# Optimization experiments

Measured on AMD Instinct MI355X. Metric: run time of the kernel, lower is better.

## Reference

```python
import jax, jax.numpy as jnp
import numpy as np
import math

B, C, H, W = 32, 256, 56, 56
M = 16            # num_frequency_mixtures
MIX = 4           # sqrt(M)
K = 8             # num_fourier_basis + 1
HID = 16
STRIDE = (1, 1)
EPS = 1e-5


def setup_inputs() -> dict:
    key = jax.random.key(0)
    ks = jax.random.split(key, 8)
    return {
        "x": jax.random.normal(ks[0], (B, C, H, W), jnp.float32),
        "fc1_w": jax.random.normal(ks[1], (HID, C), jnp.float32) * 0.08,
        "fc1_b": jnp.zeros((HID,), jnp.float32),
        "ln_g": jnp.ones((HID,), jnp.float32),
        "ln_b": jnp.zeros((HID,), jnp.float32),
        "fh_w": jax.random.normal(ks[2], (C * M * K, HID), jnp.float32) * 0.08,
        "fh_b": jnp.zeros((C * M * K,), jnp.float32),
        "basis_real": jax.random.normal(ks[3], (K, 56, 32), jnp.float32) * 0.5,
        "basis_imag": jax.random.normal(ks[4], (K, 56, 32), jnp.float32) * 0.5,
        "conv_w": jax.random.normal(ks[5], (C, C), jnp.float32) * (1.0 / math.sqrt(C)),
        "bn_g": jnp.ones((C,), jnp.float32),
        "bn_b": jnp.zeros((C,), jnp.float32),
    }


def reference(x, fc1_w, fc1_b, ln_g, ln_b, fh_w, fh_b,
              basis_real, basis_imag, conv_w, bn_g, bn_b):
    b, c, h, w = x.shape
    # --- FrequencyAttention: GAP -> fc1 -> LN -> ReLU -> fourier_head ---
    ctx = x.mean(axis=(2, 3))                          # (B, C)
    hdn = ctx @ fc1_w.T + fc1_b                        # (B, HID)
    mu = hdn.mean(-1, keepdims=True)
    var = hdn.var(-1, keepdims=True)
    hdn = (hdn - mu) / jnp.sqrt(var + EPS) * ln_g + ln_b
    hdn = jax.nn.relu(hdn)
    att = hdn @ fh_w.T + fh_b                          # (B, C*M*K)

    coeffs = jax.nn.softmax(att.reshape(b, c, M, K), axis=-1)  # (B,C,M,K)

    # --- work-canvas sizes ---
    h_out, w_out = h // STRIDE[0], w // STRIDE[1]
    h_work = math.ceil(h / MIX) * MIX                  # 56
    w_f = w // 2 + 1                                   # 29
    w_f_work = math.ceil(w_f / MIX) * MIX              # 32
    w_work = (w_f_work - 1) * 2 if w_f_work > 1 else 1 # 62

    if (h_work, w_work) != (h, w):
        x_work = jax.image.resize(x, (b, c, h_work, w_work), "bilinear")
    else:
        x_work = x

    x_ft = jnp.fft.rfft2(x_work, s=(h_work, w_work), norm="ortho")  # (B,C,Hw,Wfw) complex
    wf = x_ft.shape[-1]                                # == w_f_work
    ph, pwf = h_work // MIX, wf // MIX                 # 14, 8

    basis = jax.lax.complex(basis_real, basis_imag)    # (K, Hw, Wfw)
    basis_p = basis.reshape(K, MIX, ph, MIX, pwf).transpose(1, 3, 0, 2, 4)
    basis_p = basis_p.reshape(M, K, ph, pwf)           # (M,K,ph,pwf)

    x_ft_p = x_ft.reshape(b, c, MIX, ph, MIX, pwf).transpose(0, 2, 4, 1, 3, 5)
    x_ft_p = x_ft_p.reshape(b, M, c, ph, pwf)          # (B,M,C,ph,pwf)

    coeffs_c = jax.lax.complex(coeffs, jnp.zeros_like(coeffs))
    coeffs_p = coeffs_c.transpose(0, 2, 1, 3)          # (B,M,C,K)

    kernel = jnp.einsum("bmck,mkhw->bmchw", coeffs_p, basis_p)  # (B,M,C,ph,pwf)
    out_ft_p = x_ft_p * kernel

    out_ft = out_ft_p.reshape(b, MIX, MIX, c, ph, pwf).transpose(0, 3, 1, 4, 2, 5)
    out_ft = out_ft.reshape(b, c, h_work, wf)

    s_work = (h_work // STRIDE[0], w_work // STRIDE[1])
    y = jnp.fft.irfft2(out_ft, s=s_work, norm="ortho")  # (B,C,56,62)

    if y.shape[2:] != (h_out, w_out):
        y = jax.image.resize(y, (b, c, h_out, w_out), "bilinear")

    # --- 1x1 conv + BatchNorm (batch statistics, training-mode math) ---
    y = jnp.einsum("bchw,oc->bohw", y, conv_w)
    m = y.mean(axis=(0, 2, 3))
    v = y.var(axis=(0, 2, 3))
    y = (y - m[None, :, None, None]) / jnp.sqrt(v + EPS)[None, :, None, None]
    y = y * bn_g[None, :, None, None] + bn_b[None, :, None, None]
    return y
```

## Files before the change

### kernel.cpp

```cpp
#include <hip/hip_runtime.h>
#include <math.h>

typedef __attribute__((ext_vector_type(4))) float f32x4;
typedef __attribute__((ext_vector_type(8))) short s16x8;
typedef __attribute__((ext_vector_type(4))) short s16x4;
typedef unsigned short ushort_t;

#define MFMA16(a, b, c) __builtin_amdgcn_mfma_f32_16x16x32_bf16((a), (b), (c), 0, 0, 0)

#define WO_CTX    0u
#define WO_HDN    32768u
#define WO_BNSUM  34816u
#define WO_BNSQ   35840u
#define WO_SCALE  36864u
#define WO_SHIFT  37888u
#define WO_COEF   40960u
#define WO_BMT_H  4235264u
#define WO_BMT_L  4243456u
#define WO_FARE_H 4251648u
#define WO_FARE_L 4268032u
#define WO_FAIM_H 4284416u
#define WO_FAIM_L 4300800u
#define WO_FDRE_H 4317184u
#define WO_FDRE_L 4333568u
#define WO_FDIM_H 4349952u
#define WO_FDIM_L 4366336u
#define WO_DTT_H  4382720u
#define WO_DTT_L  4390912u
#define WO_CW_H   4399104u
#define WO_CW_L   4530176u
#define WO_YBF    4661248u
#define WO_BASRT  56041472u
#define WO_BASIT  56098816u

__device__ __forceinline__ ushort_t f2bf(float f) {
  unsigned int u = __builtin_bit_cast(unsigned int, f);
  unsigned int r = (u + 0x7fffu + ((u >> 16) & 1u)) >> 16;
  return (ushort_t)r;
}
__device__ __forceinline__ float bf2f(ushort_t h) {
  unsigned int u = ((unsigned int)h) << 16;
  return __builtin_bit_cast(float, u);
}

__device__ double bmat_val(int w, int vv) {
  const int v = vv & 31;
  const bool isI = vv >= 32;
  double accR = 0.0, accI = 0.0;
  for (int wp = 0; wp < 62; ++wp) {
    const double src = (wp + 0.5) * (56.0 / 62.0) - 0.5;
    const int w0 = (int)floor(src);
    const double f = src - (double)w0;
    const double s0 = (w0 >= 0 && w0 <= 55) ? (1.0 - f) : 0.0;
    const double s1 = (w0 + 1 >= 0 && w0 + 1 <= 55) ? f : 0.0;
    const double ssum = s0 + s1;
    double wgt = 0.0;
    if (w == w0) wgt = s0 / ssum;
    else if (w == w0 + 1) wgt = s1 / ssum;
    if (wgt != 0.0) {
      const int p = (v * wp) % 62;
      const double ang = 6.283185307179586476925286766559 * (double)p / 62.0;
      accR += wgt * cos(ang);
      accI -= wgt * sin(ang);
    }
  }
  const double nrm = 1.0 / sqrt(3472.0);
  return (isI ? accI : accR) * nrm;
}

__device__ double dt_component(int v, bool isI, int wq) {
  const double ks = 62.0 / 56.0;
  const double src = (wq + 0.5) * ks - 0.5;
  double wsum = 0.0;
  for (int wp = 0; wp < 62; ++wp) {
    const double xx = fabs(src - (double)wp) / ks;
    if (xx < 1.0) wsum += 1.0 - xx;
  }
  const double cv = (v == 0 || v == 31) ? 1.0 : 2.0;
  double accR = 0.0, accI = 0.0;
  for (int wp = 0; wp < 62; ++wp) {
    const double xx = fabs(src - (double)wp) / ks;
    if (xx >= 1.0) continue;
    const double wgt = (1.0 - xx) / wsum;
    double cc, ss;
    if (v == 0)       { cc = 1.0; ss = 0.0; }
    else if (v == 31) { cc = (wp & 1) ? -1.0 : 1.0; ss = 0.0; }
    else {
      const int p = (v * wp) % 62;
      const double ang = 6.283185307179586476925286766559 * (double)p / 62.0;
      cc = cos(ang); ss = sin(ang);
    }
    accR += wgt * cv * cc;
    accI -= wgt * cv * ss;
  }
  const double nrm = 1.0 / sqrt(3472.0);
  return (isI ? accI : accR) * nrm;
}

__device__ __forceinline__ void emit_hilo(ushort_t* hp, ushort_t* lp, int off, double val) {
  const float fv = (float)val;
  const ushort_t h = f2bf(fv);
  const float hf = bf2f(h);
  const ushort_t l = f2bf((float)(val - (double)hf));
  hp[off] = h;
  lp[off] = l;
}

__global__ void k_const(const float* __restrict__ conv_w,
                        const float* __restrict__ basR, const float* __restrict__ basI,
                        ushort_t* BmT_h, ushort_t* BmT_l,
                        ushort_t* FARe_h, ushort_t* FARe_l,
                        ushort_t* FAIm_h, ushort_t* FAIm_l,
                        ushort_t* FDRe_h, ushort_t* FDRe_l,
                        ushort_t* FDIm_h, ushort_t* FDIm_l,
                        ushort_t* DtT_h, ushort_t* DtT_l,
                        ushort_t* W_h, ushort_t* W_l,
                        float* basRT, float* basIT) {
  const int idx = blockIdx.x * 256 + threadIdx.x;
  if (idx < 4096) {
    const int vv = idx >> 6, k = idx & 63;
    const double v = (k < 56) ? bmat_val(k, vv) : 0.0;
    emit_hilo(BmT_h, BmT_l, idx, v);
  } else if (idx < 36864) {
    const int t = (idx - 4096) & 8191;
    const int which = (idx - 4096) >> 13;
    const int row = t >> 7, k = t & 127;
    double val = 0.0;
    if (row < 56 && k < 112) {
      const int h = (k < 56) ? k : k - 56;
      const double ang = 6.283185307179586476925286766559 *
                         (double)((row * h) % 56) / 56.0;
      const double c = cos(ang), s = sin(ang);
      const bool lowk = (k < 56);
      if (which == 0)      val = lowk ? c : s;
      else if (which == 1) val = lowk ? -s : c;
      else if (which == 2) val = lowk ? c : -s;
      else                 val = lowk ? s : c;
    }
    ushort_t* hp = (which == 0) ? FARe_h : (which == 1) ? FAIm_h : (which == 2) ? FDRe_h : FDIm_h;
    ushort_t* lp = (which == 0) ? FARe_l : (which == 1) ? FAIm_l : (which == 2) ? FDRe_l : FDIm_l;
    emit_hilo(hp, lp, t, val);
  } else if (idx < 40960) {
    const int t = idx - 36864;
    const int w = t >> 6, kk = t & 63;
    const double val = (w < 56) ? dt_component(kk >> 1, (kk & 1) != 0, w) : 0.0;
    emit_hilo(DtT_h, DtT_l, t, val);
  } else if (idx < 106496) {
    const int t = idx - 40960;
    emit_hilo(W_h, W_l, t, (double)conv_w[t]);
  } else if (idx < 135168) {
    const int t = idx - 106496;
    const int tt = t - (t / 14336) * 14336;
    const int m2 = t / 14336;
    const int q = tt >> 3, k = tt & 7;
    if (m2 == 0) basRT[tt] = basR[k * 1792 + q];
    else         basIT[tt] = basI[k * 1792 + q];
  }
}

__global__ __launch_bounds__(256) void k_gap(const float* __restrict__ x,
                                             float* __restrict__ ctx) {
  const int img = blockIdx.x;
  const int tid = threadIdx.x;
  const float4* p4 = (const float4*)(x + (size_t)img * 3136);
  float s = 0.f;
  for (int i = tid; i < 784; i += 256) {
    const float4 v = p4[i];
    s += v.x + v.y + v.z + v.w;
  }
  for (int off = 32; off > 0; off >>= 1) s += __shfl_down(s, off, 64);
  __shared__ float ls[4];
  if ((tid & 63) == 0) ls[tid >> 6] = s;
  __syncthreads();
  if (tid == 0) ctx[img] = (ls[0] + ls[1] + ls[2] + ls[3]) * (1.0f / 3136.0f);
}

__global__ void k_mlp(const float* __restrict__ ctx, const float* __restrict__ fc1_w,
                      const float* __restrict__ fc1_b, const float* __restrict__ ln_g,
                      const float* __restrict__ ln_b, float* __restrict__ hdn) {
  const int b = blockIdx.x;
  const int j = threadIdx.x;
  __shared__ float h[16];
  if (j < 16) {
    const float* cr = ctx + b * 256;
    const float* wr = fc1_w + j * 256;
    float acc = fc1_b[j];
    for (int c0 = 0; c0 < 256; ++c0) acc = fmaf(cr[c0], wr[c0], acc);
    h[j] = acc;
  }
  __syncthreads();
  if (j < 16) {
    float mu = 0.f, m2 = 0.f;
    for (int t = 0; t < 16; ++t) { mu += h[t]; m2 += h[t] * h[t]; }
    mu *= 0.0625f; m2 *= 0.0625f;
    const float var = m2 - mu * mu;
    const float val = (h[j] - mu) / sqrtf(var + 1e-5f) * ln_g[j] + ln_b[j];
    hdn[b * 16 + j] = fmaxf(val, 0.f);
  }
}

__global__ __launch_bounds__(256) void k_coeffs(const float* __restrict__ hdn,
                                                const float* __restrict__ fh_w,
                                                const float* __restrict__ fh_b,
                                                float* __restrict__ coeffs) {
  const int gid = blockIdx.x * 256 + threadIdx.x;
  const int b = gid >> 12;
  const int cm = gid & 4095;
  float hv[16];
  const float* hp = hdn + b * 16;
#pragma unroll
  for (int j = 0; j < 16; ++j) hv[j] = hp[j];
  const int row0 = cm * 8;
  float a[8];
  float mx = -1e30f;
#pragma unroll
  for (int k = 0; k < 8; ++k) {
    const float* wr = fh_w + (size_t)(row0 + k) * 16;
    float acc = fh_b[row0 + k];
#pragma unroll
    for (int j = 0; j < 16; ++j) acc = fmaf(hv[j], wr[j], acc);
    a[k] = acc;
    mx = fmaxf(mx, acc);
  }
  float s = 0.f;
#pragma unroll
  for (int k = 0; k < 8; ++k) { a[k] = expf(a[k] - mx); s += a[k]; }
  const float inv = 1.f / s;
  float* outp = coeffs + (size_t)gid * 8;
#pragma unroll
  for (int k = 0; k < 8; ++k) outp[k] = a[k] * inv;
}

__global__ __launch_bounds__(64) void k_fft(
    const float* __restrict__ x, const float* __restrict__ coeffs,
    const float* __restrict__ basRT, const float* __restrict__ basIT,
    const ushort_t* __restrict__ BmT_h, const ushort_t* __restrict__ BmT_l,
    const ushort_t* __restrict__ FARe_h, const ushort_t* __restrict__ FARe_l,
    const ushort_t* __restrict__ FAIm_h, const ushort_t* __restrict__ FAIm_l,
    const ushort_t* __restrict__ FDRe_h, const ushort_t* __restrict__ FDRe_l,
    const ushort_t* __restrict__ FDIm_h, const ushort_t* __restrict__ FDIm_l,
    const ushort_t* __restrict__ DtT_h, const ushort_t* __restrict__ DtT_l,
    ushort_t* __restrict__ ybf) {
  __shared__ __align__(16) ushort_t regA[4608];
  __shared__ __align__(16) ushort_t regB[4608];
  const int img = blockIdx.x;
  const int lane = threadIdx.x;
  const int col = lane & 15, quad = lane >> 4;
  const f32x4 zf = {0.f, 0.f, 0.f, 0.f};

  {
#pragma unroll
    for (int i = 0; i < 4; ++i) {
      const int t = i * 64 + lane;
      if (t < 224) {
        const int h = t >> 2, c = t & 3;
        *(unsigned int*)&regA[h * 72 + 56 + c * 2] = 0u;
      }
    }
#pragma unroll
    for (int i = 0; i < 4; ++i) {
      const int t = i * 64 + lane;
      const int r = t >> 3, c = t & 7;
      *(unsigned int*)&regB[r * 136 + 112 + c * 2] = 0u;
    }
    const float4* xp = (const float4*)(x + (size_t)img * 3136);
    for (int f = lane; f < 784; f += 64) {
      const float4 v = xp[f];
      const int h = f / 14, w4 = (f % 14) * 4;
      s16x4 p;
      p[0] = (short)f2bf(v.x); p[1] = (short)f2bf(v.y);
      p[2] = (short)f2bf(v.z); p[3] = (short)f2bf(v.w);
      *(s16x4*)&regA[h * 72 + w4] = p;
    }
  }
  __syncthreads();

#pragma unroll
  for (int mt = 0; mt < 4; ++mt) {
    const int arow = (mt * 16 + col) * 72;
    const s16x8 a0 = *(const s16x8*)&regA[arow + quad * 8];
    const s16x8 a1 = *(const s16x8*)&regA[arow + 32 + quad * 8];
    const int h0 = mt * 16 + quad * 4;
#pragma unroll
    for (int nt = 0; nt < 4; ++nt) {
      const int nrow = nt * 16 + col;
      const s16x8 bh0 = *(const s16x8*)&BmT_h[nrow * 64 + quad * 8];
      const s16x8 bl0 = *(const s16x8*)&BmT_l[nrow * 64 + quad * 8];
      const s16x8 bh1 = *(const s16x8*)&BmT_h[nrow * 64 + 32 + quad * 8];
      const s16x8 bl1 = *(const s16x8*)&BmT_l[nrow * 64 + 32 + quad * 8];
      f32x4 acc = zf;
      acc = MFMA16(a0, bh0, acc);
      acc = MFMA16(a0, bl0, acc);
      acc = MFMA16(a1, bh1, acc);
      acc = MFMA16(a1, bl1, acc);
      if (h0 < 56) {
        s16x4 p;
        p[0] = (short)f2bf(acc[0]); p[1] = (short)f2bf(acc[1]);
        p[2] = (short)f2bf(acc[2]); p[3] = (short)f2bf(acc[3]);
        const int vr = nrow & 31;
        const int kk = (nrow < 32) ? h0 : 56 + h0;
        *(s16x4*)&regB[vr * 136 + kk] = p;
      }
    }
  }
  __syncthreads();

  {
#pragma unroll
    for (int i = 0; i < 4; ++i) {
      const int t = i * 64 + lane;
      const int r = t >> 3, c = t & 7;
      *(unsigned int*)&regA[r * 136 + 112 + c * 2] = 0u;
    }
    const float* co = coeffs + (size_t)img * 128;
#pragma unroll
    for (int mt = 0; mt < 4; ++mt) {
      f32x4 accRe[2] = {zf, zf}, accIm[2] = {zf, zf};
#pragma unroll
      for (int ks = 0; ks < 4; ++ks) {
        const int aoff = (mt * 16 + col) * 128 + ks * 32 + quad * 8;
        const s16x8 aRh = *(const s16x8*)&FARe_h[aoff];
        const s16x8 aRl = *(const s16x8*)&FARe_l[aoff];
        const s16x8 aIh = *(const s16x8*)&FAIm_h[aoff];
        const s16x8 aIl = *(const s16x8*)&FAIm_l[aoff];
#pragma unroll
        for (int nt = 0; nt < 2; ++nt) {
          const s16x8 b = *(const s16x8*)&regB[(nt * 16 + col) * 136 + ks * 32 + quad * 8];
          accRe[nt] = MFMA16(aRh, b, accRe[nt]);
          accRe[nt] = MFMA16(aRl, b, accRe[nt]);
          accIm[nt] = MFMA16(aIh, b, accIm[nt]);
          accIm[nt] = MFMA16(aIl, b, accIm[nt]);
        }
      }
      const int u0 = mt * 16 + quad * 4;
      if (u0 < 56) {
#pragma unroll
        for (int nt = 0; nt < 2; ++nt) {
          const int v = nt * 16 + col;
          s16x4 pR, pI;
#pragma unroll
          for (int r = 0; r < 4; ++r) {
            const int u = u0 + r;
            const int q = u * 32 + v;
            const int m = (u / 14) * 4 + (v >> 3);
            const float4 c0 = *(const float4*)&co[m * 8];
            const float4 c1 = *(const float4*)&co[m * 8 + 4];
            const float4 br0 = *(const float4*)&basRT[q * 8];
            const float4 br1 = *(const float4*)&basRT[q * 8 + 4];
            const float4 bi0 = *(const float4*)&basIT[q * 8];
            const float4 bi1 = *(const float4*)&basIT[q * 8 + 4];
            float gr = 0.f, gi = 0.f;
            gr = fmaf(c0.x, br0.x, gr); gi = fmaf(c0.x, bi0.x, gi);
            gr = fmaf(c0.y, br0.y, gr); gi = fmaf(c0.y, bi0.y, gi);
            gr = fmaf(c0.z, br0.z, gr); gi = fmaf(c0.z, bi0.z, gi);
            gr = fmaf(c0.w, br0.w, gr); gi = fmaf(c0.w, bi0.w, gi);
            gr = fmaf(c1.x, br1.x, gr); gi = fmaf(c1.x, bi1.x, gi);
            gr = fmaf(c1.y, br1.y, gr); gi = fmaf(c1.y, bi1.y, gi);
            gr = fmaf(c1.z, br1.z, gr); gi = fmaf(c1.z, bi1.z, gi);
            gr = fmaf(c1.w, br1.w, gr); gi = fmaf(c1.w, bi1.w, gi);
            const float re = accRe[nt][r] * gr - accIm[nt][r] * gi;
            const float im = accRe[nt][r] * gi + accIm[nt][r] * gr;
            pR[r] = (short)f2bf(re);
            pI[r] = (short)f2bf(im);
          }
          *(s16x4*)&regA[v * 136 + u0] = pR;
          *(s16x4*)&regA[v * 136 + 56 + u0] = pI;
        }
      }
    }
  }
  __syncthreads();

#pragma unroll
  for (int mt = 0; mt < 4; ++mt) {
    f32x4 accRe[2] = {zf, zf}, accIm[2] = {zf, zf};
#pragma unroll
    for (int ks = 0; ks < 4; ++ks) {
      const int aoff = (mt * 16 + col) * 128 + ks * 32 + quad * 8;
      const s16x8 aRh = *(const s16x8*)&FDRe_h[aoff];
      const s16x8 aRl = *(const s16x8*)&FDRe_l[aoff];
      const s16x8 aIh = *(const s16x8*)&FDIm_h[aoff];
      const s16x8 aIl = *(const s16x8*)&FDIm_l[aoff];
#pragma unroll
      for (int nt = 0; nt < 2; ++nt) {
        const s16x8 b = *(const s16x8*)&regA[(nt * 16 + col) * 136 + ks * 32 + quad * 8];
        accRe[nt] = MFMA16(aRh, b, accRe[nt]);
        accRe[nt] = MFMA16(aRl, b, accRe[nt]);
        accIm[nt] = MFMA16(aIh, b, accIm[nt]);
        accIm[nt] = MFMA16(aIl, b, accIm[nt]);
      }
    }
    const int h0 = mt * 16 + quad * 4;
#pragma unroll
    for (int nt = 0; nt < 2; ++nt) {
      const int v = nt * 16 + col;
#pragma unroll
      for (int r = 0; r < 4; ++r) {
        const unsigned int pk = (unsigned int)f2bf(accRe[nt][r]) |
                                ((unsigned int)f2bf(accIm[nt][r]) << 16);
        *(unsigned int*)&regB[(h0 + r) * 72 + 2 * v] = pk;
      }
    }
  }
  __syncthreads();

  {
    ushort_t* yo = ybf + (size_t)img * 3136;
#pragma unroll
    for (int mt = 0; mt < 4; ++mt) {
      const int arow = (mt * 16 + col) * 72;
      const s16x8 a0 = *(const s16x8*)&regB[arow + quad * 8];
      const s16x8 a1 = *(const s16x8*)&regB[arow + 32 + quad * 8];
      const int h0 = mt * 16 + quad * 4;
#pragma unroll
      for (int nt = 0; nt < 4; ++nt) {
        const int w = nt * 16 + col;
        const s16x8 bh0 = *(const s16x8*)&DtT_h[w * 64 + quad * 8];
        const s16x8 bl0 = *(const s16x8*)&DtT_l[w * 64 + quad * 8];
        const s16x8 bh1 = *(const s16x8*)&DtT_h[w * 64 + 32 + quad * 8];
        const s16x8 bl1 = *(const s16x8*)&DtT_l[w * 64 + 32 + quad * 8];
        f32x4 acc = zf;
        acc = MFMA16(a0, bh0, acc);
        acc = MFMA16(a0, bl0, acc);
        acc = MFMA16(a1, bh1, acc);
        acc = MFMA16(a1, bl1, acc);
        if (h0 < 56 && w < 56) {
#pragma unroll
          for (int r = 0; r < 4; ++r) yo[(h0 + r) * 56 + w] = f2bf(acc[r]);
        }
      }
    }
  }
}

__global__ __launch_bounds__(256) void k_conv(const ushort_t* __restrict__ ybf,
                                              const ushort_t* __restrict__ W_h,
                                              const ushort_t* __restrict__ W_l,
                                              float* __restrict__ z) {
  const int pb = blockIdx.x;
  const int oh = blockIdx.y;
  const int b = blockIdx.z;
  const int tid = threadIdx.x;
  const int wave = tid >> 6, lane = tid & 63, col = lane & 15, quad = lane >> 4;
  const f32x4 zf = {0.f, 0.f, 0.f, 0.f};
  f32x4 acc[8][4];
#pragma unroll
  for (int mt = 0; mt < 8; ++mt)
#pragma unroll
    for (int i = 0; i < 4; ++i) acc[mt][i] = zf;

  const size_t ybase = (size_t)b * 256 * 3136;
  int p0i[4];
  bool act[4];
#pragma unroll
  for (int i = 0; i < 4; ++i) {
    p0i[i] = pb * 256 + (wave * 4 + i) * 16;
    act[i] = p0i[i] < 3136;
  }

  for (int ks = 0; ks < 8; ++ks) {
    const int c0 = ks * 32 + quad * 8;
    s16x8 bfr[4];
#pragma unroll
    for (int i = 0; i < 4; ++i) {
      if (act[i]) {
        s16x8 t;
#pragma unroll
        for (int j = 0; j < 8; ++j)
          t[j] = (short)ybf[ybase + (size_t)(c0 + j) * 3136 + p0i[i] + col];
        bfr[i] = t;
      }
    }
#pragma unroll
    for (int mt = 0; mt < 8; ++mt) {
      const int orow = oh * 128 + mt * 16 + col;
      const s16x8 ah = *(const s16x8*)&W_h[orow * 256 + ks * 32 + quad * 8];
      const s16x8 al = *(const s16x8*)&W_l[orow * 256 + ks * 32 + quad * 8];
#pragma unroll
      for (int i = 0; i < 4; ++i) {
        if (act[i]) {
          acc[mt][i] = MFMA16(ah, bfr[i], acc[mt][i]);
          acc[mt][i] = MFMA16(al, bfr[i], acc[mt][i]);
        }
      }
    }
  }

#pragma unroll
  for (int mt = 0; mt < 8; ++mt) {
#pragma unroll
    for (int i = 0; i < 4; ++i) {
      if (!act[i]) continue;
#pragma unroll
      for (int r = 0; r < 4; ++r) {
        const int o = oh * 128 + mt * 16 + quad * 4 + r;
        z[((size_t)b * 256 + o) * 3136 + p0i[i] + col] = acc[mt][i][r];
      }
    }
  }
}

__global__ __launch_bounds__(256) void k_bnsum(const float* __restrict__ z,
                                               float* __restrict__ bnsum,
                                               float* __restrict__ bnsq) {
  const int bo = blockIdx.x;
  const int tid = threadIdx.x;
  const float4* p4 = (const float4*)(z + (size_t)bo * 3136);
  float s = 0.f, s2 = 0.f;
  for (int i = tid; i < 784; i += 256) {
    const float4 v = p4[i];
    s += v.x + v.y + v.z + v.w;
    s2 += v.x * v.x + v.y * v.y + v.z * v.z + v.w * v.w;
  }
  for (int off = 32; off > 0; off >>= 1) {
    s += __shfl_down(s, off, 64);
    s2 += __shfl_down(s2, off, 64);
  }
  __shared__ float ls[8];
  if ((tid & 63) == 0) { ls[tid >> 6] = s; ls[4 + (tid >> 6)] = s2; }
  __syncthreads();
  if (tid == 0) {
    atomicAdd(bnsum + (bo & 255), ls[0] + ls[1] + ls[2] + ls[3]);
    atomicAdd(bnsq + (bo & 255), ls[4] + ls[5] + ls[6] + ls[7]);
  }
}

__global__ void k_bnstats(const float* __restrict__ bnsum, const float* __restrict__ bnsq,
                          const float* __restrict__ bn_g, const float* __restrict__ bn_b,
                          float* __restrict__ scale, float* __restrict__ shift) {
  const int o = threadIdx.x;
  if (o < 256) {
    const float N = 32.f * 3136.f;
    const float m = bnsum[o] / N;
    const float v = bnsq[o] / N - m * m;
    const float sc = bn_g[o] / sqrtf(v + 1e-5f);
    scale[o] = sc;
    shift[o] = bn_b[o] - m * sc;
  }
}

__global__ __launch_bounds__(256) void k_bnapply(float* __restrict__ z,
                                                 const float* __restrict__ scale,
                                                 const float* __restrict__ shift) {
  const size_t i = ((size_t)blockIdx.x * 256 + threadIdx.x) * 4;
  const int ch = (int)((i / 3136) & 255);
  const float sc = scale[ch], sh = shift[ch];
  float4 v = *(float4*)(z + i);
  v.x = fmaf(v.x, sc, sh);
  v.y = fmaf(v.y, sc, sh);
  v.z = fmaf(v.z, sc, sh);
  v.w = fmaf(v.w, sc, sh);
  *(float4*)(z + i) = v;
}

extern "C" void kernel_launch(void* const* d_in, const int* in_sizes, int n_in,
                              void* d_out, int out_size, void* d_ws, size_t ws_size,
                              hipStream_t stream) {
  const float* x          = (const float*)d_in[0];
  const float* fc1_w      = (const float*)d_in[1];
  const float* fc1_b      = (const float*)d_in[2];
  const float* ln_g       = (const float*)d_in[3];
  const float* ln_b       = (const float*)d_in[4];
  const float* fh_w       = (const float*)d_in[5];
  const float* fh_b       = (const float*)d_in[6];
  const float* basis_real = (const float*)d_in[7];
  const float* basis_imag = (const float*)d_in[8];
  const float* conv_w     = (const float*)d_in[9];
  const float* bn_g       = (const float*)d_in[10];
  const float* bn_b       = (const float*)d_in[11];
  float* out = (float*)d_out;
  char* ws = (char*)d_ws;
  (void)in_sizes; (void)n_in; (void)out_size; (void)ws_size;

  float* ctx   = (float*)(ws + WO_CTX);
  float* hdn   = (float*)(ws + WO_HDN);
  float* bnsum = (float*)(ws + WO_BNSUM);
  float* bnsq  = (float*)(ws + WO_BNSQ);
  float* scale = (float*)(ws + WO_SCALE);
  float* shift = (float*)(ws + WO_SHIFT);
  float* coef  = (float*)(ws + WO_COEF);
  ushort_t* BmT_h  = (ushort_t*)(ws + WO_BMT_H);
  ushort_t* BmT_l  = (ushort_t*)(ws + WO_BMT_L);
  ushort_t* FARe_h = (ushort_t*)(ws + WO_FARE_H);
  ushort_t* FARe_l = (ushort_t*)(ws + WO_FARE_L);
  ushort_t* FAIm_h = (ushort_t*)(ws + WO_FAIM_H);
  ushort_t* FAIm_l = (ushort_t*)(ws + WO_FAIM_L);
  ushort_t* FDRe_h = (ushort_t*)(ws + WO_FDRE_H);
  ushort_t* FDRe_l = (ushort_t*)(ws + WO_FDRE_L);
  ushort_t* FDIm_h = (ushort_t*)(ws + WO_FDIM_H);
  ushort_t* FDIm_l = (ushort_t*)(ws + WO_FDIM_L);
  ushort_t* DtT_h  = (ushort_t*)(ws + WO_DTT_H);
  ushort_t* DtT_l  = (ushort_t*)(ws + WO_DTT_L);
  ushort_t* W_h    = (ushort_t*)(ws + WO_CW_H);
  ushort_t* W_l    = (ushort_t*)(ws + WO_CW_L);
  ushort_t* ybf    = (ushort_t*)(ws + WO_YBF);
  float* basRT = (float*)(ws + WO_BASRT);
  float* basIT = (float*)(ws + WO_BASIT);

  hipMemsetAsync(bnsum, 0, 2048, stream);

  hipLaunchKernelGGL(k_const, dim3(528), dim3(256), 0, stream,
                     conv_w, basis_real, basis_imag,
                     BmT_h, BmT_l, FARe_h, FARe_l, FAIm_h, FAIm_l,
                     FDRe_h, FDRe_l, FDIm_h, FDIm_l, DtT_h, DtT_l, W_h, W_l,
                     basRT, basIT);
  hipLaunchKernelGGL(k_gap, dim3(8192), dim3(256), 0, stream, x, ctx);
  hipLaunchKernelGGL(k_mlp, dim3(32), dim3(64), 0, stream,
                     ctx, fc1_w, fc1_b, ln_g, ln_b, hdn);
  hipLaunchKernelGGL(k_coeffs, dim3(512), dim3(256), 0, stream, hdn, fh_w, fh_b, coef);
  hipLaunchKernelGGL(k_fft, dim3(8192), dim3(64), 0, stream,
                     x, coef, basRT, basIT,
                     BmT_h, BmT_l, FARe_h, FARe_l, FAIm_h, FAIm_l,
                     FDRe_h, FDRe_l, FDIm_h, FDIm_l, DtT_h, DtT_l, ybf);
  hipLaunchKernelGGL(k_conv, dim3(13, 2, 32), dim3(256), 0, stream, ybf, W_h, W_l, out);
  hipLaunchKernelGGL(k_bnsum, dim3(8192), dim3(256), 0, stream, out, bnsum, bnsq);
  hipLaunchKernelGGL(k_bnstats, dim3(1), dim3(256), 0, stream,
                     bnsum, bnsq, bn_g, bn_b, scale, shift);
  hipLaunchKernelGGL(k_bnapply, dim3(25088), dim3(256), 0, stream, out, scale, shift);
}
```

Baseline: 634.4 us.

## Fuse BN statistics into conv kernel and stage activations via swizzled LDS tiles

The 1x1 conv kernel now loads activation tiles with coalesced 16-byte global reads into a double-buffered, XOR-swizzled LDS tile instead of doing strided per-element gathers. It computes per-channel sum and sum-of-squares in the epilogue with shuffles and LDS atomics, which removes the separate k_bnsum pass that re-read the whole fp32 output. Tiles shrink to 64 output channels by 128 pixels, so the grid grows and occupancy may rise. In exchange the kernel gains more global atomics and extra syncthreads.

```diff
diff --git a/kernel.cpp b/kernel.cpp
--- a/kernel.cpp
+++ b/kernel.cpp
@@ -436,92 +436,126 @@
 __global__ __launch_bounds__(256) void k_conv(const ushort_t* __restrict__ ybf,
                                               const ushort_t* __restrict__ W_h,
                                               const ushort_t* __restrict__ W_l,
-                                              float* __restrict__ z) {
+                                              float* __restrict__ z,
+                                              float* __restrict__ bnsum,
+                                              float* __restrict__ bnsq) {
+  __shared__ __align__(16) ushort_t tile[2][32 * 128];
+  __shared__ float ls_sum[64];
+  __shared__ float ls_sq[64];
   const int pb = blockIdx.x;
   const int oh = blockIdx.y;
-  const int b = blockIdx.z;
+  const int b  = blockIdx.z;
   const int tid = threadIdx.x;
   const int wave = tid >> 6, lane = tid & 63, col = lane & 15, quad = lane >> 4;
   const f32x4 zf = {0.f, 0.f, 0.f, 0.f};
-  f32x4 acc[8][4];
-#pragma unroll
-  for (int mt = 0; mt < 8; ++mt)
-#pragma unroll
-    for (int i = 0; i < 4; ++i) acc[mt][i] = zf;
-
-  const size_t ybase = (size_t)b * 256 * 3136;
-  int p0i[4];
-  bool act[4];
-#pragma unroll
-  for (int i = 0; i < 4; ++i) {
-    p0i[i] = pb * 256 + (wave * 4 + i) * 16;
-    act[i] = p0i[i] < 3136;
-  }
-
+
+  if (tid < 64) { ls_sum[tid] = 0.f; ls_sq[tid] = 0.f; }
+
+  f32x4 acc[4][2];
+#pragma unroll
+  for (int mt = 0; mt < 4; ++mt)
+#pragma unroll
+    for (int i = 0; i < 2; ++i) acc[mt][i] = zf;
+
+  const int p0 = pb * 128;
+  int pL[2];
+  bool act[2];
+#pragma unroll
+  for (int i = 0; i < 2; ++i) {
+    pL[i] = (wave * 2 + i) * 16;
+    act[i] = (p0 + pL[i]) < 3136;
+  }
+  int prd[2];
+#pragma unroll
+  for (int i = 0; i < 2; ++i) prd[i] = (pL[i] + col) ^ (quad << 3);
+
+  const int sc = tid >> 3;
+  const int px8a = tid & 7;
+  const int px8b = (tid & 7) + 8;
+  const int swz = ((sc >> 3) & 3) << 3;
+  const int lda = sc * 128 + ((px8a * 8) ^ swz);
+  const int ldb = sc * 128 + ((px8b * 8) ^ swz);
+  const bool sacta = (p0 + px8a * 8) < 3136;
+  const bool sactb = (p0 + px8b * 8) < 3136;
+
+  const s16x8 zs = {0, 0, 0, 0, 0, 0, 0, 0};
+  s16x8 pfa, pfb;
+  {
+    const size_t base = (size_t)(b * 256 + sc) * 3136 + p0;
+    pfa = sacta ? *(const s16x8*)&ybf[base + px8a * 8] : zs;
+    pfb = sactb ? *(const s16x8*)&ybf[base + px8b * 8] : zs;
+  }
+
+  int buf = 0;
   for (int ks = 0; ks < 8; ++ks) {
-    const int c0 = ks * 32 + quad * 8;
-    s16x8 bfr[4];
-#pragma unroll
-    for (int i = 0; i < 4; ++i) {
+    *(s16x8*)&tile[buf][lda] = pfa;
+    *(s16x8*)&tile[buf][ldb] = pfb;
+    __syncthreads();
+    if (ks < 7) {
+      const size_t base = (size_t)(b * 256 + (ks + 1) * 32 + sc) * 3136 + p0;
+      pfa = sacta ? *(const s16x8*)&ybf[base + px8a * 8] : zs;
+      pfb = sactb ? *(const s16x8*)&ybf[base + px8b * 8] : zs;
+    }
+    s16x8 bfr[2];
+#pragma unroll
+    for (int i = 0; i < 2; ++i) {
+      bfr[i] = zs;
       if (act[i]) {
-        s16x8 t;
 #pragma unroll
         for (int j = 0; j < 8; ++j)
-          t[j] = (short)ybf[ybase + (size_t)(c0 + j) * 3136 + p0i[i] + col];
-        bfr[i] = t;
-      }
-    }
-#pragma unroll
-    for (int mt = 0; mt < 8; ++mt) {
-      const int orow = oh * 128 + mt * 16 + col;
+          bfr[i][j] = (short)tile[buf][(quad * 8 + j) * 128 + prd[i]];
+      }
+    }
+#pragma unroll
+    for (int mt = 0; mt < 4; ++mt) {
+      const int orow = oh * 64 + mt * 16 + col;
       const s16x8 ah = *(const s16x8*)&W_h[orow * 256 + ks * 32 + quad * 8];
       const s16x8 al = *(const s16x8*)&W_l[orow * 256 + ks * 32 + quad * 8];
 #pragma unroll
-      for (int i = 0; i < 4; ++i) {
+      for (int i = 0; i < 2; ++i) {
         if (act[i]) {
           acc[mt][i] = MFMA16(ah, bfr[i], acc[mt][i]);
           acc[mt][i] = MFMA16(al, bfr[i], acc[mt][i]);
         }
       }
     }
-  }
-
-#pragma unroll
-  for (int mt = 0; mt < 8; ++mt) {
-#pragma unroll
-    for (int i = 0; i < 4; ++i) {
-      if (!act[i]) continue;
-#pragma unroll
-      for (int r = 0; r < 4; ++r) {
-        const int o = oh * 128 + mt * 16 + quad * 4 + r;
-        z[((size_t)b * 256 + o) * 3136 + p0i[i] + col] = acc[mt][i][r];
-      }
-    }
-  }
-}
-
-__global__ __launch_bounds__(256) void k_bnsum(const float* __restrict__ z,
-                                               float* __restrict__ bnsum,
-                                               float* __restrict__ bnsq) {
-  const int bo = blockIdx.x;
-  const int tid = threadIdx.x;
-  const float4* p4 = (const float4*)(z + (size_t)bo * 3136);
-  float s = 0.f, s2 = 0.f;
-  for (int i = tid; i < 784; i += 256) {
-    const float4 v = p4[i];
-    s += v.x + v.y + v.z + v.w;
-    s2 += v.x * v.x + v.y * v.y + v.z * v.z + v.w * v.w;
-  }
-  for (int off = 32; off > 0; off >>= 1) {
-    s += __shfl_down(s, off, 64);
-    s2 += __shfl_down(s2, off, 64);
-  }
-  __shared__ float ls[8];
-  if ((tid & 63) == 0) { ls[tid >> 6] = s; ls[4 + (tid >> 6)] = s2; }
+    buf ^= 1;
+  }
+
+#pragma unroll
+  for (int mt = 0; mt < 4; ++mt) {
+#pragma unroll
+    for (int r = 0; r < 4; ++r) {
+      const int chl = mt * 16 + quad * 4 + r;
+      const int o = oh * 64 + chl;
+      float s = 0.f, s2 = 0.f;
+#pragma unroll
+      for (int i = 0; i < 2; ++i) {
+        if (act[i]) {
+          const float v = acc[mt][i][r];
+          s += v;
+          s2 += v * v;
+          z[((size_t)b * 256 + o) * 3136 + p0 + pL[i] + col] = v;
+        }
+      }
+      s += __shfl_xor(s, 8, 16);
+      s += __shfl_xor(s, 4, 16);
+      s += __shfl_xor(s, 2, 16);
+      s += __shfl_xor(s, 1, 16);
+      s2 += __shfl_xor(s2, 8, 16);
+      s2 += __shfl_xor(s2, 4, 16);
+      s2 += __shfl_xor(s2, 2, 16);
+      s2 += __shfl_xor(s2, 1, 16);
+      if (col == 0) {
+        atomicAdd(&ls_sum[chl], s);
+        atomicAdd(&ls_sq[chl], s2);
+      }
+    }
+  }
   __syncthreads();
-  if (tid == 0) {
-    atomicAdd(bnsum + (bo & 255), ls[0] + ls[1] + ls[2] + ls[3]);
-    atomicAdd(bnsq + (bo & 255), ls[4] + ls[5] + ls[6] + ls[7]);
+  if (tid < 64) {
+    atomicAdd(bnsum + oh * 64 + tid, ls_sum[tid]);
+    atomicAdd(bnsq + oh * 64 + tid, ls_sq[tid]);
   }
 }
 
@@ -612,8 +646,8 @@
                      x, coef, basRT, basIT,
                      BmT_h, BmT_l, FARe_h, FARe_l, FAIm_h, FAIm_l,
                      FDRe_h, FDRe_l, FDIm_h, FDIm_l, DtT_h, DtT_l, ybf);
-  hipLaunchKernelGGL(k_conv, dim3(13, 2, 32), dim3(256), 0, stream, ybf, W_h, W_l, out);
-  hipLaunchKernelGGL(k_bnsum, dim3(8192), dim3(256), 0, stream, out, bnsum, bnsq);
+  hipLaunchKernelGGL(k_conv, dim3(25, 4, 32), dim3(256), 0, stream,
+                     ybf, W_h, W_l, out, bnsum, bnsq);
   hipLaunchKernelGGL(k_bnstats, dim3(1), dim3(256), 0, stream,
                      bnsum, bnsq, bn_g, bn_b, scale, shift);
   hipLaunchKernelGGL(k_bnapply, dim3(25088), dim3(256), 0, stream, out, scale, shift);
```

Measured after the change: 629.6 us. About the same (-0.8%).
